# Kernel optimization log

Measured on AMD Instinct MI355X. Metric: run time of the kernel, lower is better.

## Reference

```python
import jax, jax.numpy as jnp
import numpy as np

B, S, D, E, F = 2, 1024, 1024, 14, 2048

def setup_inputs() -> dict:
    key = jax.random.key(0)
    k0, k1, k2, k3 = jax.random.split(key, 4)
    h = jax.random.normal(k0, (B, S, D), jnp.float32)
    gate_w = jax.random.normal(k1, (E, D), jnp.float32) * 0.02
    # kaiming-uniform-ish scale for expert weights
    w1 = jax.random.normal(k2, (E, D, F), jnp.float32) * (1.0 / np.sqrt(D).astype(np.float32))
    b1 = jnp.zeros((E, F), jnp.float32)
    w2 = jax.random.normal(k3, (E, F, D), jnp.float32) * (1.0 / np.sqrt(F).astype(np.float32))
    b2 = jnp.zeros((E, D), jnp.float32)
    return {"h": h, "gate_w": gate_w, "w1": w1, "b1": b1, "w2": w2, "b2": b2}

def reference(h, gate_w, w1, b1, w2, b2):
    # Eval-mode forward (no expert dropout, router_step=None, return_aux=False path)
    Bb, Ss, Dd = h.shape
    x = h.reshape(Bb * Ss, Dd)                       # (N, D)
    logits = x @ gate_w.T                            # (N, E)
    probs = jax.nn.softmax(logits, axis=-1)
    top2_p, top2_i = jax.lax.top_k(probs, 2)         # (N, 2)
    w = top2_p / jnp.maximum(top2_p.sum(-1, keepdims=True), 1e-10)
    # dense all-experts FFN
    hh = jnp.einsum('nd,edf->nef', x, w1) + b1       # (N, E, F)
    hh = jax.nn.gelu(hh, approximate=False)          # torch F.gelu default = exact erf
    all_out = jnp.einsum('nef,efd->ned', hh, w2) + b2  # (N, E, D)
    n = jnp.arange(x.shape[0])
    out0 = all_out[n, top2_i[:, 0]]                  # (N, D)
    out1 = all_out[n, top2_i[:, 1]]
    moe_out = w[:, 0:1] * out0 + w[:, 1:2] * out1
    result = jnp.clip(x + moe_out, -100.0, 100.0).reshape(Bb, Ss, Dd)
    return result
```

## Files before the change

### kernel.cpp

```cpp
#include <hip/hip_runtime.h>
#include <cstdint>
#include <cstddef>

#define NTOK 2048
#define DDIM 1024
#define FDIM 2048
#define NEXP 14
#define MAXT 2048
#define BM   160

typedef __attribute__((ext_vector_type(8))) short short8;
typedef __attribute__((ext_vector_type(4))) float floatx4;

__device__ __forceinline__ unsigned pack2bf(float lo, float hi) {
    unsigned a = __float_as_uint(lo), b = __float_as_uint(hi);
    return ((a + 0x8000u) >> 16) | ((b + 0x8000u) & 0xffff0000u);
}
__device__ __forceinline__ unsigned short f2bf1(float f) {
    return (unsigned short)((__float_as_uint(f) + 0x8000u) >> 16);
}

__device__ __forceinline__ void glds16(const void* g, void* lds) {
    __builtin_amdgcn_global_load_lds((const __attribute__((address_space(1))) unsigned*)g,
                                     (__attribute__((address_space(3))) unsigned*)lds, 16, 0, 0);
}

__device__ __forceinline__ int bswz(int n) { return ((n >> 2) ^ n ^ (n >> 4)) & 7; }

#define SBAR() __builtin_amdgcn_sched_barrier(0)

__global__ __launch_bounds__(256) void cvtx_kernel(const float* __restrict__ x,
                                                   unsigned short* __restrict__ xb,
                                                   int* __restrict__ cnt) {
    if (blockIdx.x == 0 && threadIdx.x < NEXP) cnt[threadIdx.x] = 0;
    const size_t i = ((size_t)blockIdx.x * 256 + threadIdx.x) * 8;
    float4 a = *(const float4*)(x + i);
    float4 b = *(const float4*)(x + i + 4);
    uint4 u;
    u.x = pack2bf(a.x, a.y); u.y = pack2bf(a.z, a.w);
    u.z = pack2bf(b.x, b.y); u.w = pack2bf(b.z, b.w);
    *(uint4*)(xb + i) = u;
}

__global__ __launch_bounds__(256) void gate_kernel(
    const float* __restrict__ x, const float* __restrict__ gw,
    int* __restrict__ cnt, int* __restrict__ lists, float* __restrict__ wt)
{
    const int wave = threadIdx.x >> 6, lane = threadIdx.x & 63;
    const int n = blockIdx.x * 4 + wave;
    float part[NEXP];
#pragma unroll
    for (int e = 0; e < NEXP; ++e) part[e] = 0.f;
    const float4* xr = (const float4*)(x + (size_t)n * DDIM);
#pragma unroll
    for (int kk = 0; kk < 4; ++kk) {
        const float4 xv = xr[kk * 64 + lane];
#pragma unroll
        for (int e = 0; e < NEXP; ++e) {
            const float4 g = ((const float4*)(gw + e * DDIM))[kk * 64 + lane];
            part[e] = fmaf(xv.x, g.x, fmaf(xv.y, g.y, fmaf(xv.z, g.z, fmaf(xv.w, g.w, part[e]))));
        }
    }
#pragma unroll
    for (int e = 0; e < NEXP; ++e) {
        float v = part[e];
        for (int off = 32; off; off >>= 1) v += __shfl_xor(v, off);
        part[e] = v;
    }
    int i0 = 0; float l0 = part[0];
#pragma unroll
    for (int e = 1; e < NEXP; ++e) if (part[e] > l0) { l0 = part[e]; i0 = e; }
    int i1 = -1; float l1 = -3.0e38f;
#pragma unroll
    for (int e = 0; e < NEXP; ++e) if (e != i0 && part[e] > l1) { l1 = part[e]; i1 = e; }
    if (lane == 0) {
        const float r  = __expf(l1 - l0);
        wt[2 * n]     = 1.f / (1.f + r);
        wt[2 * n + 1] = r / (1.f + r);
        int p0 = atomicAdd(&cnt[i0], 1); lists[i0 * MAXT + p0] = 2 * n;
        int p1 = atomicAdd(&cnt[i1], 1); lists[i1 * MAXT + p1] = 2 * n + 1;
    }
}

#define MAXJOBS 40
__global__ void jobs_kernel(const int* __restrict__ cnt, int* __restrict__ job_e,
                            int* __restrict__ job_mt, int* __restrict__ njobs) {
    if (threadIdx.x == 0) {
        int J = 0;
        for (int e = 0; e < NEXP; ++e) {
            const int m = (cnt[e] + BM - 1) / BM;
            for (int i = 0; i < m; ++i) { job_e[J] = e; job_mt[J] = i; ++J; }
        }
        njobs[0] = J;
    }
}

#define LOADB(dst, kbase, STRIDE) {                                           \
    _Pragma("unroll") for (int jj = 0; jj < 8; ++jj)                          \
        dst[jj] = *(const floatx4*)(bG + (size_t)((kbase) + kg * 8 + jj) * (STRIDE)); }

#define WRITEB(src, buf) {                                                    \
    _Pragma("unroll") for (int nn = 0; nn < 4; ++nn) {                        \
        const int n_ = n4 + nn, slot_ = kg ^ bswz(n_);                        \
        uint4 u_;                                                             \
        u_.x = pack2bf(src[0][nn], src[1][nn]); u_.y = pack2bf(src[2][nn], src[3][nn]); \
        u_.z = pack2bf(src[4][nn], src[5][nn]); u_.w = pack2bf(src[6][nn], src[7][nn]); \
        *(uint4*)&Bs[buf][n_ * 64 + slot_ * 8] = u_; } }

#define STAGEA(buf, koff) {                                                   \
    _Pragma("unroll") for (int q = 0; q < 5; ++q)                             \
        glds16(aGp[q] + (koff), &As[buf][(wave * 40 + q * 8) * 64]); }

#define COMPUTE(buf) {                                                        \
    _Pragma("unroll") for (int ks = 0; ks < 2; ++ks) {                        \
        const int c_ = ks * 4 + lq;                                           \
        short8 af[5], bf[4];                                                  \
        _Pragma("unroll") for (int ii = 0; ii < 5; ++ii) {                    \
            const int r_ = wm + ii * 16 + lrow;                               \
            af[ii] = *(const short8*)&As[buf][r_ * 64 + ((c_ ^ (r_ & 7)) * 8)]; } \
        _Pragma("unroll") for (int jn = 0; jn < 4; ++jn) {                    \
            const int n_ = wn + jn * 16 + lrow;                               \
            bf[jn] = *(const short8*)&Bs[buf][n_ * 64 + ((c_ ^ bswz(n_)) * 8)]; } \
        __builtin_amdgcn_s_setprio(1);                                        \
        _Pragma("unroll") for (int ii = 0; ii < 5; ++ii)                      \
            _Pragma("unroll") for (int jn = 0; jn < 4; ++jn)                  \
                acc[ii][jn] = __builtin_amdgcn_mfma_f32_16x16x32_bf16(af[ii], bf[jn], acc[ii][jn], 0, 0, 0); \
        __builtin_amdgcn_s_setprio(0); } }

#define STEADY(i, curbuf, brv_c, brv_n, STRIDE) {                             \
    STAGEA((curbuf) ^ 1, ((i) + 1) * 64);                                     \
    WRITEB(brv_c, (curbuf) ^ 1);                                              \
    SBAR();                                                                   \
    LOADB(brv_n, ((i) + 2) * 64, STRIDE);                                     \
    SBAR();                                                                   \
    COMPUTE(curbuf);                                                          \
    asm volatile("s_waitcnt vmcnt(8) lgkmcnt(0)" ::: "memory");               \
    __builtin_amdgcn_s_barrier(); }

__global__ __launch_bounds__(256, 2) void gemm1_kernel(
    const unsigned short* __restrict__ xb, const float* __restrict__ w1,
    const float* __restrict__ b1, const int* __restrict__ cnt,
    const int* __restrict__ lists, const int* __restrict__ job_e,
    const int* __restrict__ job_mt, const int* __restrict__ njobs,
    unsigned short* __restrict__ hh)
{
    const int id = blockIdx.x;
    const int j  = (id >> 7) * 8 + (id & 7);
    const int nt = (id >> 3) & 15;
    if (j >= njobs[0]) return;
    const int e = job_e[j], mt = job_mt[j];
    const int count = cnt[e];
    const int* list = lists + e * MAXT + mt * BM;
    const int mloc = min(BM, count - mt * BM);

    __shared__ __align__(16) unsigned short As[2][BM * 64];
    __shared__ __align__(16) unsigned short Bs[2][128 * 64];

    const int t = threadIdx.x, lane = t & 63, wave = t >> 6;
    const int lrow = lane & 15, lq = lane >> 4;
    const int wm = (wave & 1) * 80, wn = (wave >> 1) * 64;

    const int achk = (lane & 7) ^ (lane >> 3);
    const unsigned short* aGp[5];
#pragma unroll
    for (int q = 0; q < 5; ++q) {
        const int r = wave * 40 + q * 8 + (lane >> 3);
        aGp[q] = xb + (size_t)(list[min(r, mloc - 1)] >> 1) * DDIM + achk * 8;
    }

    const int n4 = (t & 31) * 4, kg = t >> 5;
    const float* bG = w1 + (size_t)e * DDIM * FDIM + nt * 128 + n4;

    floatx4 acc[5][4];
#pragma unroll
    for (int ii = 0; ii < 5; ++ii)
#pragma unroll
        for (int jn = 0; jn < 4; ++jn) acc[ii][jn] = (floatx4)0.f;

    floatx4 brvA[8], brvB[8];

    STAGEA(0, 0);
    SBAR();
    LOADB(brvB, 0, FDIM);
    WRITEB(brvB, 0);
    SBAR();
    LOADB(brvA, 64, FDIM);
    asm volatile("s_waitcnt vmcnt(8) lgkmcnt(0)" ::: "memory");
    __builtin_amdgcn_s_barrier();

#pragma unroll 1
    for (int it = 0; it < 7; ++it) {
        const int i = it * 2;
        STEADY(i, 0, brvA, brvB, FDIM);
        STEADY(i + 1, 1, brvB, brvA, FDIM);
    }
    STAGEA(1, 15 * 64);
    WRITEB(brvA, 1);
    SBAR();
    COMPUTE(0);
    asm volatile("s_waitcnt vmcnt(0) lgkmcnt(0)" ::: "memory");
    __builtin_amdgcn_s_barrier();
    COMPUTE(1);

#pragma unroll
    for (int jn = 0; jn < 4; ++jn) {
        const int n = nt * 128 + wn + jn * 16 + lrow;
        const float bias = b1[e * FDIM + n];
#pragma unroll
        for (int ii = 0; ii < 5; ++ii) {
#pragma unroll
            for (int r = 0; r < 4; ++r) {
                const int m = wm + ii * 16 + lq * 4 + r;
                if (m < mloc) {
                    const int pp = list[m];
                    float v = acc[ii][jn][r] + bias;
                    v = 0.5f * v * (1.0f + erff(v * 0.70710678118654752f));
                    hh[(size_t)pp * FDIM + n] = f2bf1(v);
                }
            }
        }
    }
}

__global__ __launch_bounds__(256, 2) void gemm2_kernel(
    const unsigned short* __restrict__ hh, const float* __restrict__ w2,
    const float* __restrict__ b2, const int* __restrict__ cnt,
    const int* __restrict__ lists, const int* __restrict__ job_e,
    const int* __restrict__ job_mt, const int* __restrict__ njobs,
    const float* __restrict__ wt, float* __restrict__ out0, float* __restrict__ out1)
{
    const int id = blockIdx.x;
    const int j  = (id >> 6) * 8 + (id & 7);
    const int nt = (id >> 3) & 7;
    if (j >= njobs[0]) return;
    const int e = job_e[j], mt = job_mt[j];
    const int count = cnt[e];
    const int* list = lists + e * MAXT + mt * BM;
    const int mloc = min(BM, count - mt * BM);

    __shared__ __align__(16) unsigned short As[2][BM * 64];
    __shared__ __align__(16) unsigned short Bs[2][128 * 64];

    const int t = threadIdx.x, lane = t & 63, wave = t >> 6;
    const int lrow = lane & 15, lq = lane >> 4;
    const int wm = (wave & 1) * 80, wn = (wave >> 1) * 64;

    const int achk = (lane & 7) ^ (lane >> 3);
    const unsigned short* aGp[5];
#pragma unroll
    for (int q = 0; q < 5; ++q) {
        const int r = wave * 40 + q * 8 + (lane >> 3);
        aGp[q] = hh + (size_t)list[min(r, mloc - 1)] * FDIM + achk * 8;
    }

    const int n4 = (t & 31) * 4, kg = t >> 5;
    const float* bG = w2 + (size_t)e * FDIM * DDIM + nt * 128 + n4;

    floatx4 acc[5][4];
#pragma unroll
    for (int ii = 0; ii < 5; ++ii)
#pragma unroll
        for (int jn = 0; jn < 4; ++jn) acc[ii][jn] = (floatx4)0.f;

    floatx4 brvA[8], brvB[8];

    STAGEA(0, 0);
    SBAR();
    LOADB(brvB, 0, DDIM);
    WRITEB(brvB, 0);
    SBAR();
    LOADB(brvA, 64, DDIM);
    asm volatile("s_waitcnt vmcnt(8) lgkmcnt(0)" ::: "memory");
    __builtin_amdgcn_s_barrier();

#pragma unroll 1
    for (int it = 0; it < 15; ++it) {
        const int i = it * 2;
        STEADY(i, 0, brvA, brvB, DDIM);
        STEADY(i + 1, 1, brvB, brvA, DDIM);
    }
    STAGEA(1, 31 * 64);
    WRITEB(brvA, 1);
    SBAR();
    COMPUTE(0);
    asm volatile("s_waitcnt vmcnt(0) lgkmcnt(0)" ::: "memory");
    __builtin_amdgcn_s_barrier();
    COMPUTE(1);

#pragma unroll
    for (int jn = 0; jn < 4; ++jn) {
        const int n = nt * 128 + wn + jn * 16 + lrow;
        const float bias = b2[e * DDIM + n];
#pragma unroll
        for (int ii = 0; ii < 5; ++ii) {
#pragma unroll
            for (int r = 0; r < 4; ++r) {
                const int m = wm + ii * 16 + lq * 4 + r;
                if (m < mloc) {
                    const int pp = list[m];
                    const int tok = pp >> 1;
                    const float v = (acc[ii][jn][r] + bias) * wt[pp];
                    float* dst = (pp & 1) ? out1 : out0;
                    dst[(size_t)tok * DDIM + n] = v;
                }
            }
        }
    }
}

__global__ __launch_bounds__(256) void finalize_kernel(
    const float* __restrict__ x, const float* __restrict__ o1,
    float* __restrict__ out)
{
    const size_t i = ((size_t)blockIdx.x * 256 + threadIdx.x) * 4;
    float4 xv = *(const float4*)(x + i);
    float4 a  = *(const float4*)(out + i);
    float4 b  = *(const float4*)(o1 + i);
    float4 r;
    r.x = fminf(fmaxf(xv.x + a.x + b.x, -100.f), 100.f);
    r.y = fminf(fmaxf(xv.y + a.y + b.y, -100.f), 100.f);
    r.z = fminf(fmaxf(xv.z + a.z + b.z, -100.f), 100.f);
    r.w = fminf(fmaxf(xv.w + a.w + b.w, -100.f), 100.f);
    *(float4*)(out + i) = r;
}

extern "C" void kernel_launch(void* const* d_in, const int* in_sizes, int n_in,
                              void* d_out, int out_size, void* d_ws, size_t ws_size,
                              hipStream_t stream) {
    const float* h  = (const float*)d_in[0];
    const float* gw = (const float*)d_in[1];
    const float* w1 = (const float*)d_in[2];
    const float* b1 = (const float*)d_in[3];
    const float* w2 = (const float*)d_in[4];
    const float* b2 = (const float*)d_in[5];
    float* out = (float*)d_out;

    char* ws = (char*)d_ws;
    int*   cnt    = (int*)ws;
    int*   lists  = (int*)(ws + 256);
    float* wt     = (float*)(ws + 114944);
    int*   job_e  = (int*)(ws + 131328);
    int*   job_mt = (int*)(ws + 131840);
    int*   njobs  = (int*)(ws + 132352);
    unsigned short* xb = (unsigned short*)(ws + 262144);
    float* o1     = (float*)(ws + 262144 + 4194304);
    unsigned short* hhb = (unsigned short*)(ws + 262144 + 4194304 + 8388608);

    cvtx_kernel<<<NTOK * DDIM / (256 * 8), 256, 0, stream>>>(h, xb, cnt);
    gate_kernel<<<NTOK / 4, 256, 0, stream>>>(h, gw, cnt, lists, wt);
    jobs_kernel<<<1, 64, 0, stream>>>(cnt, job_e, job_mt, njobs);
    gemm1_kernel<<<5 * 128, 256, 0, stream>>>(xb, w1, b1, cnt, lists, job_e, job_mt, njobs, hhb);
    gemm2_kernel<<<5 * 64, 256, 0, stream>>>(hhb, w2, b2, cnt, lists, job_e, job_mt, njobs, wt, out, o1);
    finalize_kernel<<<NTOK * DDIM / (256 * 4), 256, 0, stream>>>(h, o1, out);
}
```

Before: 419.2 us.

## Pre-retile expert weights to bf16 tiled layout and stream B via LDS DMA

Adds two retile kernels that convert the fp32 expert weights w1/w2 to bf16 on every call, storing them in a K-chunked, tile-contiguous layout. The grouped GEMMs then stage B tiles with direct global-to-LDS 16-byte loads, the same way as A, instead of loading fp32 into registers, packing and writing to LDS. This removes the per-block conversion and register staging work and simplifies the pipeline to one barrier per step. In exchange it adds a full extra pass over both weight tensors (read fp32, write bf16) and needs about 147 MB of workspace. If the workspace is smaller, the old kernels are used instead.

```diff
diff --git a/kernel.cpp b/kernel.cpp
--- a/kernel.cpp
+++ b/kernel.cpp
@@ -95,6 +95,234 @@
     }
 }
 
+
+__global__ __launch_bounds__(256) void retile1_kernel(const float* __restrict__ w1,
+                                                      unsigned short* __restrict__ wb1) {
+    __shared__ unsigned short lb[8 * 2048];
+    const int bid = blockIdx.x;
+    const int e = bid >> 7, r8 = bid & 127;
+    const int kt = r8 >> 3, c = r8 & 7;
+    const int t = threadIdx.x;
+    const float* src = w1 + ((size_t)e * 1024 + r8 * 8) * 2048;
+#pragma unroll
+    for (int jr = 0; jr < 8; ++jr) {
+        float4 v0 = *(const float4*)(src + (size_t)jr * 2048 + t * 8);
+        float4 v1 = *(const float4*)(src + (size_t)jr * 2048 + t * 8 + 4);
+        uint4 u;
+        u.x = pack2bf(v0.x, v0.y); u.y = pack2bf(v0.z, v0.w);
+        u.z = pack2bf(v1.x, v1.y); u.w = pack2bf(v1.z, v1.w);
+        *(uint4*)&lb[jr * 2048 + t * 8] = u;
+    }
+    __syncthreads();
+#pragma unroll
+    for (int o = 0; o < 8; ++o) {
+        const int f = t + o * 256;
+        const int nt = f >> 7, n = f & 127;
+        uint4 u;
+        u.x = lb[0 * 2048 + f] | ((unsigned)lb[1 * 2048 + f] << 16);
+        u.y = lb[2 * 2048 + f] | ((unsigned)lb[3 * 2048 + f] << 16);
+        u.z = lb[4 * 2048 + f] | ((unsigned)lb[5 * 2048 + f] << 16);
+        u.w = lb[6 * 2048 + f] | ((unsigned)lb[7 * 2048 + f] << 16);
+        *(uint4*)&wb1[(((size_t)(e * 16 + nt) * 16 + kt) * 8192) + (c * 128 + n) * 8] = u;
+    }
+}
+
+__global__ __launch_bounds__(256) void retile2_kernel(const float* __restrict__ w2,
+                                                      unsigned short* __restrict__ wb2) {
+    __shared__ unsigned short lb[8 * 1024];
+    const int bid = blockIdx.x;
+    const int e = bid >> 8, r8 = bid & 255;
+    const int kt = r8 >> 3, c = r8 & 7;
+    const int t = threadIdx.x;
+    const float* src = w2 + ((size_t)e * 2048 + r8 * 8) * 1024;
+#pragma unroll
+    for (int jr = 0; jr < 8; ++jr) {
+        float4 v0 = *(const float4*)(src + (size_t)jr * 1024 + t * 4);
+        uint2 u;
+        u.x = pack2bf(v0.x, v0.y); u.y = pack2bf(v0.z, v0.w);
+        *(uint2*)&lb[jr * 1024 + t * 4] = u;
+    }
+    __syncthreads();
+#pragma unroll
+    for (int o = 0; o < 4; ++o) {
+        const int f = t + o * 256;
+        const int nt = f >> 7, n = f & 127;
+        uint4 u;
+        u.x = lb[0 * 1024 + f] | ((unsigned)lb[1 * 1024 + f] << 16);
+        u.y = lb[2 * 1024 + f] | ((unsigned)lb[3 * 1024 + f] << 16);
+        u.z = lb[4 * 1024 + f] | ((unsigned)lb[5 * 1024 + f] << 16);
+        u.w = lb[6 * 1024 + f] | ((unsigned)lb[7 * 1024 + f] << 16);
+        *(uint4*)&wb2[(((size_t)(e * 8 + nt) * 32 + kt) * 8192) + (c * 128 + n) * 8] = u;
+    }
+}
+
+#define STAGEA(buf, koff) {                                                   \
+    _Pragma("unroll") for (int q = 0; q < 5; ++q)                             \
+        glds16(aGp[q] + (koff), &As[buf][(wave * 40 + q * 8) * 64]); }
+
+#define STAGEB(buf, step) {                                                   \
+    _Pragma("unroll") for (int q = 0; q < 4; ++q)                             \
+        glds16(bsrc[q] + (size_t)(step) * 8192, &Bs[buf][(wave * 4 + q) * 512]); }
+
+#define COMPUTE_N(buf) {                                                      \
+    _Pragma("unroll") for (int ks = 0; ks < 2; ++ks) {                        \
+        const int c_ = ks * 4 + lq;                                           \
+        short8 af[5], bf[4];                                                  \
+        _Pragma("unroll") for (int ii = 0; ii < 5; ++ii) {                    \
+            const int r_ = wm + ii * 16 + lrow;                               \
+            af[ii] = *(const short8*)&As[buf][r_ * 64 + ((c_ ^ (r_ & 7)) * 8)]; } \
+        _Pragma("unroll") for (int jn = 0; jn < 4; ++jn) {                    \
+            const int n_ = wn + jn * 16 + lrow;                               \
+            bf[jn] = *(const short8*)&Bs[buf][c_ * 1024 + n_ * 8]; }          \
+        __builtin_amdgcn_s_setprio(1);                                        \
+        _Pragma("unroll") for (int ii = 0; ii < 5; ++ii)                      \
+            _Pragma("unroll") for (int jn = 0; jn < 4; ++jn)                  \
+                acc[ii][jn] = __builtin_amdgcn_mfma_f32_16x16x32_bf16(af[ii], bf[jn], acc[ii][jn], 0, 0, 0); \
+        __builtin_amdgcn_s_setprio(0); } }
+
+__global__ __launch_bounds__(256, 2) void gemm1_kernel(
+    const unsigned short* __restrict__ xb, const unsigned short* __restrict__ wb1,
+    const float* __restrict__ b1, const int* __restrict__ cnt,
+    const int* __restrict__ lists, const int* __restrict__ job_e,
+    const int* __restrict__ job_mt, const int* __restrict__ njobs,
+    unsigned short* __restrict__ hh)
+{
+    const int nt = blockIdx.x, j = blockIdx.y;
+    if (j >= njobs[0]) return;
+    const int e = job_e[j], mt = job_mt[j];
+    const int count = cnt[e];
+    const int* list = lists + e * MAXT + mt * BM;
+    const int mloc = min(BM, count - mt * BM);
+
+    __shared__ __align__(16) unsigned short As[2][BM * 64];
+    __shared__ __align__(16) unsigned short Bs[2][8192];
+
+    const int t = threadIdx.x, lane = t & 63, wave = t >> 6;
+    const int lrow = lane & 15, lq = lane >> 4;
+    const int wm = (wave & 1) * 80, wn = (wave >> 1) * 64;
+
+    const int achk = (lane & 7) ^ (lane >> 3);
+    const unsigned short* aGp[5];
+#pragma unroll
+    for (int q = 0; q < 5; ++q) {
+        const int r = wave * 40 + q * 8 + (lane >> 3);
+        aGp[q] = xb + (size_t)(list[min(r, mloc - 1)] >> 1) * DDIM + achk * 8;
+    }
+    const unsigned short* bP = wb1 + ((size_t)(e * 16 + nt) * 16) * 8192;
+    const unsigned short* bsrc[4];
+#pragma unroll
+    for (int q = 0; q < 4; ++q) bsrc[q] = bP + (wave * 4 + q) * 512 + lane * 8;
+
+    floatx4 acc[5][4];
+#pragma unroll
+    for (int ii = 0; ii < 5; ++ii)
+#pragma unroll
+        for (int jn = 0; jn < 4; ++jn) acc[ii][jn] = (floatx4)0.f;
+
+    STAGEA(0, 0); STAGEB(0, 0);
+    __syncthreads();
+#pragma unroll 1
+    for (int i = 0; i < 15; ++i) {
+        const int buf = i & 1;
+        STAGEA(buf ^ 1, (i + 1) * 64);
+        STAGEB(buf ^ 1, i + 1);
+        COMPUTE_N(buf);
+        __syncthreads();
+    }
+    COMPUTE_N(1);
+
+#pragma unroll
+    for (int jn = 0; jn < 4; ++jn) {
+        const int n = nt * 128 + wn + jn * 16 + lrow;
+        const float bias = b1[e * FDIM + n];
+#pragma unroll
+        for (int ii = 0; ii < 5; ++ii) {
+#pragma unroll
+            for (int r = 0; r < 4; ++r) {
+                const int m = wm + ii * 16 + lq * 4 + r;
+                if (m < mloc) {
+                    const int pp = list[m];
+                    float v = acc[ii][jn][r] + bias;
+                    v = 0.5f * v * (1.0f + erff(v * 0.70710678118654752f));
+                    hh[(size_t)pp * FDIM + n] = f2bf1(v);
+                }
+            }
+        }
+    }
+}
+
+__global__ __launch_bounds__(256, 2) void gemm2_kernel(
+    const unsigned short* __restrict__ hh, const unsigned short* __restrict__ wb2,
+    const float* __restrict__ b2, const int* __restrict__ cnt,
+    const int* __restrict__ lists, const int* __restrict__ job_e,
+    const int* __restrict__ job_mt, const int* __restrict__ njobs,
+    const float* __restrict__ wt, float* __restrict__ out0, float* __restrict__ out1)
+{
+    const int nt = blockIdx.x, j = blockIdx.y;
+    if (j >= njobs[0]) return;
+    const int e = job_e[j], mt = job_mt[j];
+    const int count = cnt[e];
+    const int* list = lists + e * MAXT + mt * BM;
+    const int mloc = min(BM, count - mt * BM);
+
+    __shared__ __align__(16) unsigned short As[2][BM * 64];
+    __shared__ __align__(16) unsigned short Bs[2][8192];
+
+    const int t = threadIdx.x, lane = t & 63, wave = t >> 6;
+    const int lrow = lane & 15, lq = lane >> 4;
+    const int wm = (wave & 1) * 80, wn = (wave >> 1) * 64;
+
+    const int achk = (lane & 7) ^ (lane >> 3);
+    const unsigned short* aGp[5];
+#pragma unroll
+    for (int q = 0; q < 5; ++q) {
+        const int r = wave * 40 + q * 8 + (lane >> 3);
+        aGp[q] = hh + (size_t)list[min(r, mloc - 1)] * FDIM + achk * 8;
+    }
+    const unsigned short* bP = wb2 + ((size_t)(e * 8 + nt) * 32) * 8192;
+    const unsigned short* bsrc[4];
+#pragma unroll
+    for (int q = 0; q < 4; ++q) bsrc[q] = bP + (wave * 4 + q) * 512 + lane * 8;
+
+    floatx4 acc[5][4];
+#pragma unroll
+    for (int ii = 0; ii < 5; ++ii)
+#pragma unroll
+        for (int jn = 0; jn < 4; ++jn) acc[ii][jn] = (floatx4)0.f;
+
+    STAGEA(0, 0); STAGEB(0, 0);
+    __syncthreads();
+#pragma unroll 1
+    for (int i = 0; i < 31; ++i) {
+        const int buf = i & 1;
+        STAGEA(buf ^ 1, (i + 1) * 64);
+        STAGEB(buf ^ 1, i + 1);
+        COMPUTE_N(buf);
+        __syncthreads();
+    }
+    COMPUTE_N(1);
+
+#pragma unroll
+    for (int jn = 0; jn < 4; ++jn) {
+        const int n = nt * 128 + wn + jn * 16 + lrow;
+        const float bias = b2[e * DDIM + n];
+#pragma unroll
+        for (int ii = 0; ii < 5; ++ii) {
+#pragma unroll
+            for (int r = 0; r < 4; ++r) {
+                const int m = wm + ii * 16 + lq * 4 + r;
+                if (m < mloc) {
+                    const int pp = list[m];
+                    const int tok = pp >> 1;
+                    const float v = (acc[ii][jn][r] + bias) * wt[pp];
+                    float* dst = (pp & 1) ? out1 : out0;
+                    dst[(size_t)tok * DDIM + n] = v;
+                }
+            }
+        }
+    }
+}
+
 #define LOADB(dst, kbase, STRIDE) {                                           \
     _Pragma("unroll") for (int jj = 0; jj < 8; ++jj)                          \
         dst[jj] = *(const floatx4*)(bG + (size_t)((kbase) + kg * 8 + jj) * (STRIDE)); }
@@ -107,11 +335,7 @@
         u_.z = pack2bf(src[4][nn], src[5][nn]); u_.w = pack2bf(src[6][nn], src[7][nn]); \
         *(uint4*)&Bs[buf][n_ * 64 + slot_ * 8] = u_; } }
 
-#define STAGEA(buf, koff) {                                                   \
-    _Pragma("unroll") for (int q = 0; q < 5; ++q)                             \
-        glds16(aGp[q] + (koff), &As[buf][(wave * 40 + q * 8) * 64]); }
-
-#define COMPUTE(buf) {                                                        \
+#define COMPUTE_F(buf) {                                                      \
     _Pragma("unroll") for (int ks = 0; ks < 2; ++ks) {                        \
         const int c_ = ks * 4 + lq;                                           \
         short8 af[5], bf[4];                                                  \
@@ -133,11 +357,11 @@
     SBAR();                                                                   \
     LOADB(brv_n, ((i) + 2) * 64, STRIDE);                                     \
     SBAR();                                                                   \
-    COMPUTE(curbuf);                                                          \
+    COMPUTE_F(curbuf);                                                        \
     asm volatile("s_waitcnt vmcnt(8) lgkmcnt(0)" ::: "memory");               \
     __builtin_amdgcn_s_barrier(); }
 
-__global__ __launch_bounds__(256, 2) void gemm1_kernel(
+__global__ __launch_bounds__(256, 2) void gemm1_fb(
     const unsigned short* __restrict__ xb, const float* __restrict__ w1,
     const float* __restrict__ b1, const int* __restrict__ cnt,
     const int* __restrict__ lists, const int* __restrict__ job_e,
@@ -167,7 +391,6 @@
         const int r = wave * 40 + q * 8 + (lane >> 3);
         aGp[q] = xb + (size_t)(list[min(r, mloc - 1)] >> 1) * DDIM + achk * 8;
     }
-
     const int n4 = (t & 31) * 4, kg = t >> 5;
     const float* bG = w1 + (size_t)e * DDIM * FDIM + nt * 128 + n4;
 
@@ -178,7 +401,6 @@
         for (int jn = 0; jn < 4; ++jn) acc[ii][jn] = (floatx4)0.f;
 
     floatx4 brvA[8], brvB[8];
-
     STAGEA(0, 0);
     SBAR();
     LOADB(brvB, 0, FDIM);
@@ -187,7 +409,6 @@
     LOADB(brvA, 64, FDIM);
     asm volatile("s_waitcnt vmcnt(8) lgkmcnt(0)" ::: "memory");
     __builtin_amdgcn_s_barrier();
-
 #pragma unroll 1
     for (int it = 0; it < 7; ++it) {
         const int i = it * 2;
@@ -197,10 +418,10 @@
     STAGEA(1, 15 * 64);
     WRITEB(brvA, 1);
     SBAR();
-    COMPUTE(0);
+    COMPUTE_F(0);
     asm volatile("s_waitcnt vmcnt(0) lgkmcnt(0)" ::: "memory");
     __builtin_amdgcn_s_barrier();
-    COMPUTE(1);
+    COMPUTE_F(1);
 
 #pragma unroll
     for (int jn = 0; jn < 4; ++jn) {
@@ -222,7 +443,7 @@
     }
 }
 
-__global__ __launch_bounds__(256, 2) void gemm2_kernel(
+__global__ __launch_bounds__(256, 2) void gemm2_fb(
     const unsigned short* __restrict__ hh, const float* __restrict__ w2,
     const float* __restrict__ b2, const int* __restrict__ cnt,
     const int* __restrict__ lists, const int* __restrict__ job_e,
@@ -252,7 +473,6 @@
         const int r = wave * 40 + q * 8 + (lane >> 3);
         aGp[q] = hh + (size_t)list[min(r, mloc - 1)] * FDIM + achk * 8;
     }
-
     const int n4 = (t & 31) * 4, kg = t >> 5;
     const float* bG = w2 + (size_t)e * FDIM * DDIM + nt * 128 + n4;
 
@@ -263,7 +483,6 @@
         for (int jn = 0; jn < 4; ++jn) acc[ii][jn] = (floatx4)0.f;
 
     floatx4 brvA[8], brvB[8];
-
     STAGEA(0, 0);
     SBAR();
     LOADB(brvB, 0, DDIM);
@@ -272,7 +491,6 @@
     LOADB(brvA, 64, DDIM);
     asm volatile("s_waitcnt vmcnt(8) lgkmcnt(0)" ::: "memory");
     __builtin_amdgcn_s_barrier();
-
 #pragma unroll 1
     for (int it = 0; it < 15; ++it) {
         const int i = it * 2;
@@ -282,10 +500,10 @@
     STAGEA(1, 31 * 64);
     WRITEB(brvA, 1);
     SBAR();
-    COMPUTE(0);
+    COMPUTE_F(0);
     asm volatile("s_waitcnt vmcnt(0) lgkmcnt(0)" ::: "memory");
     __builtin_amdgcn_s_barrier();
-    COMPUTE(1);
+    COMPUTE_F(1);
 
 #pragma unroll
     for (int jn = 0; jn < 4; ++jn) {
@@ -342,14 +560,24 @@
     int*   job_e  = (int*)(ws + 131328);
     int*   job_mt = (int*)(ws + 131840);
     int*   njobs  = (int*)(ws + 132352);
-    unsigned short* xb = (unsigned short*)(ws + 262144);
-    float* o1     = (float*)(ws + 262144 + 4194304);
-    unsigned short* hhb = (unsigned short*)(ws + 262144 + 4194304 + 8388608);
+    unsigned short* xb  = (unsigned short*)(ws + 262144);
+    float* o1           = (float*)(ws + 4456448);
+    unsigned short* hhb = (unsigned short*)(ws + 12845056);
+    unsigned short* wb1 = (unsigned short*)(ws + 29622272);
+    unsigned short* wb2 = (unsigned short*)(ws + 88342528);
 
     cvtx_kernel<<<NTOK * DDIM / (256 * 8), 256, 0, stream>>>(h, xb, cnt);
     gate_kernel<<<NTOK / 4, 256, 0, stream>>>(h, gw, cnt, lists, wt);
     jobs_kernel<<<1, 64, 0, stream>>>(cnt, job_e, job_mt, njobs);
-    gemm1_kernel<<<5 * 128, 256, 0, stream>>>(xb, w1, b1, cnt, lists, job_e, job_mt, njobs, hhb);
-    gemm2_kernel<<<5 * 64, 256, 0, stream>>>(hhb, w2, b2, cnt, lists, job_e, job_mt, njobs, wt, out, o1);
+
+    if (ws_size >= 147062784ull) {
+        retile2_kernel<<<NEXP * 256, 256, 0, stream>>>(w2, wb2);
+        retile1_kernel<<<NEXP * 128, 256, 0, stream>>>(w1, wb1);
+        gemm1_kernel<<<dim3(FDIM / 128, MAXJOBS), 256, 0, stream>>>(xb, wb1, b1, cnt, lists, job_e, job_mt, njobs, hhb);
+        gemm2_kernel<<<dim3(DDIM / 128, MAXJOBS), 256, 0, stream>>>(hhb, wb2, b2, cnt, lists, job_e, job_mt, njobs, wt, out, o1);
+    } else {
+        gemm1_fb<<<5 * 128, 256, 0, stream>>>(xb, w1, b1, cnt, lists, job_e, job_mt, njobs, hhb);
+        gemm2_fb<<<5 * 64, 256, 0, stream>>>(hhb, w2, b2, cnt, lists, job_e, job_mt, njobs, wt, out, o1);
+    }
     finalize_kernel<<<NTOK * DDIM / (256 * 4), 256, 0, stream>>>(h, o1, out);
 }
```

After: 460.6 us. +9.9%, slower.
